# Kernel optimization log

Hardware: AMD Instinct MI355X
Metric: run time of the kernel (lower is better)

Reference implementation:

```python
import jax, jax.numpy as jnp
import numpy as np
from jax import lax

D_MODEL = 512
INPUT_DIM = 64
D_INNER = 1024      # expand * d_model
D_STATE = 128
NHEADS = 16         # d_inner // headdim (headdim = ssm_state//num_heads = 64)
HEADDIM = 64
D_CONV = 4
CONV_DIM = D_INNER + 2 * D_STATE          # 1280 (ngroups=1)
D_IN_PROJ = 2 * D_INNER + 2 * D_STATE + NHEADS  # 2320
BATCH = 2
SEQ = 1024
MASK_RATIO = 0.75
EPS = 1e-5


def setup_inputs() -> dict:
    key = jax.random.key(0)
    ks = jax.random.split(key, 14)
    s = lambda fan: 1.0 / np.sqrt(fan)
    return {
        "x": jax.random.normal(ks[0], (BATCH, SEQ, INPUT_DIM), jnp.float32),
        "conv_emb_w": jax.random.normal(ks[1], (D_MODEL, INPUT_DIM, 3), jnp.float32) * s(INPUT_DIM * 3),
        "conv_emb_b": jax.random.normal(ks[2], (D_MODEL,), jnp.float32) * 0.02,
        "cls_token": jax.random.normal(ks[3], (1, 1, D_MODEL), jnp.float32) * 0.02,
        "in_proj_w": jax.random.normal(ks[4], (D_IN_PROJ, D_MODEL), jnp.float32) * s(D_MODEL),
        "conv1d_w": jax.random.normal(ks[5], (CONV_DIM, 1, D_CONV), jnp.float32) * s(D_CONV),
        "conv1d_b": jax.random.normal(ks[6], (CONV_DIM,), jnp.float32) * 0.02,
        "dt_bias": jax.random.uniform(ks[7], (NHEADS,), jnp.float32, -4.0, 0.0),
        "A_log": jnp.log(jax.random.uniform(ks[8], (NHEADS,), jnp.float32, 1.0, 16.0)),
        "D": jax.random.normal(ks[9], (NHEADS,), jnp.float32),
        "rms_w": jnp.ones((D_INNER,), jnp.float32),
        "out_proj_w": jax.random.normal(ks[10], (D_MODEL, D_INNER), jnp.float32) * s(D_INNER),
        "ln_g": jnp.ones((D_MODEL,), jnp.float32),
        "ln_b": jnp.zeros((D_MODEL,), jnp.float32),
    }


def _forward(x, conv_emb_w, conv_emb_b, cls_token, in_proj_w, conv1d_w, conv1d_b,
             dt_bias, A_log, D, rms_w, out_proj_w, ln_g, ln_b):
    b = x.shape[0]
    # ---- conv embedding: Conv1d(k=3, pad=1) over time ----
    xe = lax.conv_general_dilated(x.transpose(0, 2, 1), conv_emb_w, (1,), [(1, 1)],
                                  dimension_numbers=("NCH", "OIH", "NCH"))
    xe = (xe + conv_emb_b[None, :, None]).transpose(0, 2, 1)  # (b, L, d_model)
    # ---- append CLS token at end ----
    h = jnp.concatenate([xe, jnp.broadcast_to(cls_token, (b, 1, D_MODEL))], axis=1)
    L = h.shape[1]
    # ---- Mamba2 block ----
    zxbcdt = jnp.einsum("bld,ed->ble", h, in_proj_w)  # (b, L, 2320)
    z = zxbcdt[..., :D_INNER]
    xBC = zxbcdt[..., D_INNER:D_INNER + CONV_DIM]
    dt = jax.nn.softplus(zxbcdt[..., -NHEADS:] + dt_bias)  # (b, L, h)
    # causal depthwise conv (pad left d_conv-1) + SiLU
    xBC = lax.conv_general_dilated(xBC.transpose(0, 2, 1), conv1d_w, (1,), [(D_CONV - 1, 0)],
                                   dimension_numbers=("NCH", "OIH", "NCH"),
                                   feature_group_count=CONV_DIM)
    xBC = jax.nn.silu((xBC + conv1d_b[None, :, None]).transpose(0, 2, 1))  # (b, L, 1280)
    x_in = xBC[..., :D_INNER].reshape(b, L, NHEADS, HEADDIM)   # (b, L, h, p)
    B = xBC[..., D_INNER:D_INNER + D_STATE]                     # (b, L, n)
    C = xBC[..., D_INNER + D_STATE:]                            # (b, L, n)
    A = -jnp.exp(A_log)                                         # (h,)
    dA = jnp.exp(dt * A)                                        # (b, L, h)
    # selective state-space scan; state (b, h, p, n)
    def step(state, inp):
        x_t, dt_t, B_t, C_t, dA_t = inp  # (b,h,p) (b,h) (b,n) (b,n) (b,h)
        state = state * dA_t[:, :, None, None] + \
            (dt_t[:, :, None] * x_t)[..., None] * B_t[:, None, None, :]
        y_t = jnp.einsum("bhpn,bn->bhp", state, C_t)
        return state, y_t
    s0 = jnp.zeros((b, NHEADS, HEADDIM, D_STATE), x.dtype)
    _, ys = lax.scan(step, s0, (x_in.transpose(1, 0, 2, 3), dt.transpose(1, 0, 2),
                                B.transpose(1, 0, 2), C.transpose(1, 0, 2),
                                dA.transpose(1, 0, 2)))
    y = ys.transpose(1, 0, 2, 3) + D[None, None, :, None] * x_in  # (b, L, h, p)
    y = y.reshape(b, L, D_INNER)
    # gated RMSNorm: gate first, then normalize
    y = y * jax.nn.silu(z)
    y = y * lax.rsqrt(jnp.mean(y * y, axis=-1, keepdims=True) + EPS) * rms_w
    out = jnp.einsum("ble,de->bld", y, out_proj_w)  # (b, L, d_model)
    # ---- LayerNorm ----
    mu = jnp.mean(out, axis=-1, keepdims=True)
    var = jnp.mean((out - mu) ** 2, axis=-1, keepdims=True)
    out = (out - mu) * lax.rsqrt(var + EPS) * ln_g + ln_b
    return out


def reference(x, conv_emb_w, conv_emb_b, cls_token, in_proj_w, conv1d_w, conv1d_b,
              dt_bias, A_log, D, rms_w, out_proj_w, ln_g, ln_b):
    out = _forward(x, conv_emb_w, conv_emb_b, cls_token, in_proj_w, conv1d_w, conv1d_b,
                   dt_bias, A_log, D, rms_w, out_proj_w, ln_g, ln_b)
    b = out.shape[0]
    cls = out[:, -1:, :]
    body = out[:, :-1, :]                      # (b, SEQ, d)
    len_keep = int(SEQ * (1 - MASK_RATIO))     # 256
    noise = jax.random.uniform(jax.random.fold_in(jax.random.key(0), 1), (b, SEQ))
    ids_shuffle = jnp.argsort(noise, axis=1)
    ids_restore = jnp.argsort(ids_shuffle, axis=1)
    ids_keep = ids_shuffle[:, :len_keep]
    x_masked = jnp.take_along_axis(body, ids_keep[:, :, None], axis=1)
    mask = jnp.where(jnp.arange(SEQ)[None, :] < len_keep, 0.0, 1.0)
    mask = jnp.take_along_axis(jnp.broadcast_to(mask, (b, SEQ)), ids_restore, axis=1)
    x_out = jnp.concatenate([x_masked, cls], axis=1)  # (b, len_keep+1, d)
    return (x_out, mask, ids_restore, ids_keep)
```

## Files before the change

### kernel.cpp

```cpp
#include <hip/hip_runtime.h>
#include <hip/hip_bf16.h>
#include <stdint.h>

#define LTOK  1025
#define NROWS 2050
#define DM    512
#define DIN   1024
#define DST   128
#define NHEAD 16
#define HDIM  64
#define CDIM  1280
#define EPROJ 2320
#define QC    64
#define NCH   17

#define O_RIDX   0
#define O_CB     1024
#define O_CLS    1536
#define O_C1B    2048
#define O_DTB    3328
#define O_ALOG   3344
#define O_DV     3360
#define O_RMSW   3376
#define O_LNG    4400
#define O_LNB    4912
#define O_CW     5440
#define O_IPW    103744
#define O_OPW    1291584
#define O_C1W    1815872
#define O_CX     1820992
#define O_ZX     1952064
#define O_XBC    6708064
#define O_DT     9332064
#define O_LGA    9364864
#define O_Y      9397664
#define O_H      9397664
#define O_X3     10447264
#define O_OUTG   11496864
#define O_SL     11760032
#define O_CLA    16216480
#define O_SL2    16251296
#define O_KEEP   18479520
#define O_OUTP   18480128

#define OO_MASK 263168
#define OO_IDR  265216
#define OO_IDK  267264

typedef __attribute__((ext_vector_type(8))) short short8;
typedef __attribute__((ext_vector_type(8))) unsigned short ushortx8;
typedef __attribute__((ext_vector_type(4))) short shortx4;
typedef __attribute__((ext_vector_type(4))) float floatx4;

__device__ __forceinline__ short f2bs(float f) {
  union { float f; uint32_t u; } v; v.f = f;
  uint32_t r = (v.u + 0x7FFFu + ((v.u >> 16) & 1u)) >> 16;
  return (short)r;
}
__device__ __forceinline__ float bf2f(uint16_t u) {
  return __uint_as_float(((uint32_t)u) << 16);
}

struct InPtrs { const void* p[14]; };

__device__ __forceinline__ uint32_t rotl32(uint32_t v, int d) {
  return (v << d) | (v >> (32 - d));
}
__device__ void threefry2x32(uint32_t k0, uint32_t k1, uint32_t c0, uint32_t c1,
                             uint32_t& o0, uint32_t& o1) {
  uint32_t ks0 = k0, ks1 = k1, ks2 = 0x1BD11BDAu ^ k0 ^ k1;
  uint32_t x0 = c0 + ks0, x1 = c1 + ks1;
#define TF_R4(a,b,c,d) \
  x0 += x1; x1 = rotl32(x1,a); x1 ^= x0; \
  x0 += x1; x1 = rotl32(x1,b); x1 ^= x0; \
  x0 += x1; x1 = rotl32(x1,c); x1 ^= x0; \
  x0 += x1; x1 = rotl32(x1,d); x1 ^= x0;
  TF_R4(13,15,26,6)  x0 += ks1; x1 += ks2 + 1u;
  TF_R4(17,29,16,24) x0 += ks2; x1 += ks0 + 2u;
  TF_R4(13,15,26,6)  x0 += ks0; x1 += ks1 + 3u;
  TF_R4(17,29,16,24) x0 += ks1; x1 += ks2 + 4u;
  TF_R4(13,15,26,6)  x0 += ks2; x1 += ks0 + 5u;
#undef TF_R4
  o0 = x0; o1 = x1;
}

__device__ int detect_is_f32(const uint32_t* w, int nelem) {
  int nw = nelem / 2; if (nw > 16) nw = 16;
  int insane = 0, lozero = 0, anynz = 0;
  for (int i = 0; i < nw; ++i) {
    uint32_t word = w[i];
    if (word != 0u) anynz = 1;
    uint32_t lo = word & 0xffffu;
    if (lo == 0u) { lozero++; continue; }
    float v = __uint_as_float(lo << 16);
    float a = fabsf(v);
    if (!(a >= 1e-8f && a <= 1e4f)) insane++;
  }
  if (insane >= 2) return 1;
  if (lozero == nw && anynz) return 1;
  return 0;
}

__global__ __launch_bounds__(256) void k_convert(InPtrs ptrs, float* ws,
                                                 float* out, int* rowidx) {
  static const int sizes[13] = {98304, 512, 512, 1187840, 5120, 1280,
                                16, 16, 16, 1024, 524288, 512, 512};
  static const int offs[13]  = {O_CW, O_CB, O_CLS, O_IPW, O_C1W, O_C1B,
                                O_DTB, O_ALOG, O_DV, O_RMSW, O_OPW, O_LNG, O_LNB};
  static const int isbf[13]  = {1,0,0,1,0,0,0,0,0,0,1,0,0};
  int t = blockIdx.y;
  int tid = threadIdx.x;

  if (t >= 14) {
    int b = t - 14;
    int idx = blockIdx.x;
    if (idx > 1024) return;
    if (idx == 1024) {
      const uint32_t* cp = (const uint32_t*)ptrs.p[3];
      __shared__ int cf;
      if (tid == 0) cf = detect_is_f32(cp, 512);
      __syncthreads();
      uint16_t* hout = (uint16_t*)(ws + O_H);
      for (int cch = tid; cch < DM; cch += 256) {
        float v = cf ? ((const float*)cp)[cch] : bf2f(((const uint16_t*)cp)[cch]);
        hout[((long)(b * LTOK + 1024)) * DM + cch] = (uint16_t)f2bs(v);
      }
      return;
    }
    const uint32_t* xp = (const uint32_t*)ptrs.p[0];
    __shared__ int xf;
    if (tid == 0) xf = detect_is_f32(xp, 131072);
    __syncthreads();
    if (tid < 192) {
      int i = tid / 3, k = tid % 3;
      int tt = idx + k - 1;
      float v = 0.f;
      if (tt >= 0 && tt < 1024) {
        long src = ((long)(b * 1024 + tt)) * 64 + i;
        v = xf ? ((const float*)xp)[src] : bf2f(((const uint16_t*)xp)[src]);
      }
      ((uint16_t*)(ws + O_X3))[((long)(b * 1024 + idx)) * 192 + tid] = (uint16_t)f2bs(v);
    }
    return;
  }

  if (t == 13) {
    int bx = blockIdx.x;
    if (bx < 512 || bx >= 544) return;
    int rb = bx - 512;
    int seg = rb & 15, b = rb >> 4;
    uint8_t* keep = (uint8_t*)(ws + O_KEEP);
    __shared__ float vals[1024];
    uint32_t fk0, fk1;
    threefry2x32(0u, 0u, 0u, 1u, fk0, fk1);
#pragma unroll
    for (int k = 0; k < 4; ++k) {
      int i = tid + k * 256;
      uint32_t o0, o1;
      threefry2x32(fk0, fk1, 0u, (uint32_t)(b * 1024 + i), o0, o1);
      uint32_t bits = o0 ^ o1;
      vals[i] = __uint_as_float((bits >> 9) | 0x3f800000u) - 1.0f;
    }
    __syncthreads();
    int tg = seg * 64 + (tid >> 2);
    int qq = tid & 3;
    float v = vals[tg];
    int r = 0;
    int j0 = qq * 256;
    for (int it = 0; it < 256; ++it) {
      int j = j0 + ((it + qq * 8) & 255);
      float vj = vals[j];
      r += (vj < v || (vj == v && j < tg)) ? 1 : 0;
    }
    r += __shfl_xor(r, 1, 64);
    r += __shfl_xor(r, 2, 64);
    if (qq == 0) {
      out[OO_IDR + b * 1024 + tg] = (float)r;
      out[OO_MASK + b * 1024 + tg] = (r < 256) ? 0.0f : 1.0f;
      keep[b * LTOK + tg] = (r < 256) ? 1 : 0;
      if (r < 256) {
        out[OO_IDK + b * 256 + r] = (float)tg;
        rowidx[b * 257 + r] = b * LTOK + tg;
      }
      if (tg == 0) {
        rowidx[b * 257 + 256] = b * LTOK + 1024;
        keep[b * LTOK + 1024] = 1;
      }
    }
    return;
  }

  int n = sizes[t];
  const uint32_t* w = (const uint32_t*)ptrs.p[t + 1];
  __shared__ int sf;
  if (tid == 0) sf = detect_is_f32(w, n);
  __syncthreads();
  int base = (blockIdx.x * 256 + tid) * 4;
  if (base >= n) return;
  if (isbf[t]) {
    ushort4 o;
    if (sf) {
      const float4 vv = *(const float4*)((const float*)w + base);
      o.x = (uint16_t)f2bs(vv.x); o.y = (uint16_t)f2bs(vv.y);
      o.z = (uint16_t)f2bs(vv.z); o.w = (uint16_t)f2bs(vv.w);
    } else {
      const uint32_t* s = w + (base >> 1);
      uint32_t w0 = s[0], w1 = s[1];
      o.x = (uint16_t)(w0 & 0xffffu); o.y = (uint16_t)(w0 >> 16);
      o.z = (uint16_t)(w1 & 0xffffu); o.w = (uint16_t)(w1 >> 16);
    }
    *(ushort4*)((uint16_t*)(ws + offs[t]) + base) = o;
  } else {
    float* dst = ws + offs[t];
    if (sf) {
      *(float4*)(dst + base) = *(const float4*)((const float*)w + base);
    } else {
      const uint32_t* s = w + (base >> 1);
      uint32_t w0 = s[0], w1 = s[1];
      float4 o;
      o.x = __uint_as_float((w0 & 0xffffu) << 16);
      o.y = __uint_as_float(w0 & 0xffff0000u);
      o.z = __uint_as_float((w1 & 0xffffu) << 16);
      o.w = __uint_as_float(w1 & 0xffff0000u);
      *(float4*)(dst + base) = o;
    }
  }
}

__global__ __launch_bounds__(256) void k_cgemm(const uint16_t* __restrict__ A,
                                               const uint16_t* __restrict__ Bw,
                                               uint16_t* __restrict__ H,
                                               const float* __restrict__ bias) {
  __shared__ __align__(16) short sA[64 * 200];
  __shared__ __align__(16) short sB[64 * 200];
  int tid = threadIdx.x;
  int lane = tid & 63, w = tid >> 6;
  int lm = lane & 15, q = lane >> 4;
  int bm = blockIdx.y * 64, bn = blockIdx.x * 64;

#pragma unroll
  for (int it = 0; it < 6; ++it) {
    int li = it * 256 + tid;
    int row = li / 24, col = (li % 24) * 8;
    ushortx8 av = *(const ushortx8*)(A + (long)(bm + row) * 192 + col);
    *(ushortx8*)&sA[row * 200 + col] = av;
    ushortx8 bv = *(const ushortx8*)(Bw + (long)(bn + row) * 192 + col);
    *(ushortx8*)&sB[row * 200 + col] = bv;
  }
  __syncthreads();

  floatx4 acc[4] = {};
#pragma unroll
  for (int kb = 0; kb < 6; ++kb) {
    short8 a = *(const short8*)&sA[(w * 16 + lm) * 200 + kb * 32 + q * 8];
#pragma unroll
    for (int ct = 0; ct < 4; ++ct) {
      short8 b = *(const short8*)&sB[(ct * 16 + lm) * 200 + kb * 32 + q * 8];
      acc[ct] = __builtin_amdgcn_mfma_f32_16x16x32_bf16(a, b, acc[ct], 0, 0, 0);
    }
  }
#pragma unroll
  for (int reg = 0; reg < 4; ++reg) {
    int r = bm + w * 16 + q * 4 + reg;
    long crow = (long)((r >> 10) * LTOK + (r & 1023));
#pragma unroll
    for (int ct = 0; ct < 4; ++ct) {
      int cc = bn + ct * 16 + lm;
      H[crow * DM + cc] = (uint16_t)f2bs(acc[ct][reg] + bias[cc]);
    }
  }
}

__global__ __launch_bounds__(256) void k_ogemm(const uint16_t* __restrict__ A,
                                               const uint16_t* __restrict__ Bw,
                                               float* __restrict__ OUTP) {
  __shared__ __align__(16) short sA[64 * 264];
  __shared__ __align__(16) short sB[64 * 264];
  int tid = threadIdx.x;
  int lane = tid & 63, w = tid >> 6;
  int lm = lane & 15, q = lane >> 4;
  int bm = blockIdx.y * 64, bn = blockIdx.x * 64;
  int kbase = blockIdx.z * 256;

#pragma unroll
  for (int it = 0; it < 8; ++it) {
    int li = it * 256 + tid;
    int row = li >> 5, col = (li & 31) * 8;
    int gm = bm + row;
    ushortx8 av = {0,0,0,0,0,0,0,0};
    if (gm < 514) av = *(const ushortx8*)(A + (long)gm * 1024 + kbase + col);
    *(ushortx8*)&sA[row * 264 + col] = av;
    ushortx8 bv = *(const ushortx8*)(Bw + (long)(bn + row) * 1024 + kbase + col);
    *(ushortx8*)&sB[row * 264 + col] = bv;
  }
  __syncthreads();

  floatx4 acc[4] = {};
#pragma unroll
  for (int kb = 0; kb < 8; ++kb) {
    short8 a = *(const short8*)&sA[(w * 16 + lm) * 264 + kb * 32 + q * 8];
#pragma unroll
    for (int ct = 0; ct < 4; ++ct) {
      short8 b = *(const short8*)&sB[(ct * 16 + lm) * 264 + kb * 32 + q * 8];
      acc[ct] = __builtin_amdgcn_mfma_f32_16x16x32_bf16(a, b, acc[ct], 0, 0, 0);
    }
  }
  float* op = OUTP + (long)blockIdx.z * 263168;
#pragma unroll
  for (int reg = 0; reg < 4; ++reg) {
    int r = bm + w * 16 + q * 4 + reg;
    if (r < 514) {
#pragma unroll
      for (int ct = 0; ct < 4; ++ct)
        op[(long)r * 512 + bn + ct * 16 + lm] = acc[ct][reg];
    }
  }
}

__global__ __launch_bounds__(256) void k_bgemm(
    const void* __restrict__ A, const uint16_t* __restrict__ Bw,
    void* __restrict__ C, const float* __restrict__ bias,
    const int* __restrict__ rowmap, int M, int N, int K, int ldc,
    int cmode, int abf, int obf) {
  __shared__ __align__(16) short sA[2][128 * 40];
  __shared__ __align__(16) short sB[2][128 * 40];
  int tid = threadIdx.x;
  int lane = tid & 63, w = tid >> 6;
  int lm = lane & 15, q = lane >> 4;
  int wm = (w >> 1) * 64, wn = (w & 1) * 64;
  int bm = blockIdx.y * 128, bn = blockIdx.x * 128;
  int gz = gridDim.z;
  int Ks = K / gz;
  int kbase = blockIdx.z * Ks;
  int nk = Ks >> 5;

  int srow[4], scol[4];
  long aoff[4]; bool aok[4]; long boff[4]; bool bok[4];
#pragma unroll
  for (int it = 0; it < 4; ++it) {
    int e4 = (tid + it * 256) * 4;
    srow[it] = e4 >> 5; scol[it] = e4 & 31;
    int gm = bm + srow[it];
    aok[it] = gm < M;
    aoff[it] = aok[it] ? (long)(rowmap ? rowmap[gm] : gm) * K : 0;
    int gn = bn + srow[it];
    bok[it] = gn < N;
    boff[it] = bok[it] ? (long)gn * K : 0;
  }

  auto gload = [&](int kt, float4* vaf, ushort4* vau, ushort4* vb) {
    int kc = kbase + kt * 32;
#pragma unroll
    for (int it = 0; it < 4; ++it) {
      if (abf) {
        if (aok[it]) vau[it] = *(const ushort4*)((const uint16_t*)A + aoff[it] + kc + scol[it]);
        else { vau[it].x = 0; vau[it].y = 0; vau[it].z = 0; vau[it].w = 0; }
      } else {
        vaf[it] = aok[it] ? *(const float4*)((const float*)A + aoff[it] + kc + scol[it])
                          : make_float4(0.f, 0.f, 0.f, 0.f);
      }
      if (bok[it]) vb[it] = *(const ushort4*)(Bw + boff[it] + kc + scol[it]);
      else { vb[it].x = 0; vb[it].y = 0; vb[it].z = 0; vb[it].w = 0; }
    }
  };
  auto sstore = [&](int buf, const float4* vaf, const ushort4* vau, const ushort4* vb) {
#pragma unroll
    for (int it = 0; it < 4; ++it) {
      if (abf)
        *(ushort4*)&sA[buf][srow[it] * 40 + scol[it]] = vau[it];
      else
        *(shortx4*)&sA[buf][srow[it] * 40 + scol[it]] =
            shortx4{f2bs(vaf[it].x), f2bs(vaf[it].y), f2bs(vaf[it].z), f2bs(vaf[it].w)};
      *(ushort4*)&sB[buf][srow[it] * 40 + scol[it]] = vb[it];
    }
  };

  floatx4 acc[4][4] = {};
  float4 vaf[4], naf[4];
  ushort4 vau[4], nau[4], vb[4], nb[4];

  gload(0, vaf, vau, vb);
  sstore(0, vaf, vau, vb);
  for (int kt = 0; kt < nk; ++kt) {
    int cur = kt & 1;
    if (kt + 1 < nk) gload(kt + 1, naf, nau, nb);
    __syncthreads();
    short8 afrag[4], bfrag[4];
#pragma unroll
    for (int i = 0; i < 4; ++i)
      afrag[i] = *(const short8*)&sA[cur][(wm + i * 16 + lm) * 40 + q * 8];
#pragma unroll
    for (int j = 0; j < 4; ++j)
      bfrag[j] = *(const short8*)&sB[cur][(wn + j * 16 + lm) * 40 + q * 8];
#pragma unroll
    for (int i = 0; i < 4; ++i)
#pragma unroll
      for (int j = 0; j < 4; ++j)
        acc[i][j] = __builtin_amdgcn_mfma_f32_16x16x32_bf16(afrag[i], bfrag[j], acc[i][j], 0, 0, 0);
    if (kt + 1 < nk) sstore(1 - cur, naf, nau, nb);
  }

#pragma unroll
  for (int i = 0; i < 4; ++i) {
    int rowl = wm + i * 16 + q * 4;
#pragma unroll
    for (int reg = 0; reg < 4; ++reg) {
      int r = bm + rowl + reg;
      if (r >= M) continue;
      long crow = cmode ? (long)((r >> 10) * LTOK + (r & 1023)) : (long)r;
#pragma unroll
      for (int j = 0; j < 4; ++j) {
        int ccol = bn + wn + j * 16 + lm;
        if (ccol < N) {
          float v = acc[i][j][reg];
          if (gz > 1) {
            atomicAdd(&((float*)C)[crow * ldc + ccol], v);
          } else {
            if (bias) v += bias[ccol];
            if (obf) ((uint16_t*)C)[crow * ldc + ccol] = (uint16_t)f2bs(v);
            else ((float*)C)[crow * ldc + ccol] = v;
          }
        }
      }
    }
  }
}

__global__ __launch_bounds__(256) void k_conv1d(const uint16_t* __restrict__ zx,
                                                const float* __restrict__ w,
                                                const float* __restrict__ bias,
                                                uint16_t* __restrict__ xbc,
                                                const float* __restrict__ dtb,
                                                const float* __restrict__ alog,
                                                float* __restrict__ dt,
                                                float* __restrict__ lga) {
  long rp_ = blockIdx.x;
  if (rp_ >= NROWS) {
    int idx = (int)(rp_ - NROWS) * 256 + threadIdx.x;
    if (idx < NROWS * NHEAD) {
      int rr = idx >> 4, h = idx & 15;
      float xv = bf2f(zx[(long)rr * EPROJ + (EPROJ - NHEAD) + h]) + dtb[h];
      float dtv = (xv > 20.f) ? xv : log1pf(expf(xv));
      dt[idx] = dtv;
      lga[idx] = dtv * (-expf(alog[h]));
    }
    return;
  }
  {
    int xcd = (int)(rp_ & 7), slot = (int)(rp_ >> 3);
    rp_ = (xcd < 2) ? (long)xcd * 257 + slot
                    : (long)514 + (long)(xcd - 2) * 256 + slot;
  }
  long r = rp_;
  int b = (int)(r / LTOK), t = (int)(r % LTOK);
  for (int c4 = threadIdx.x * 4; c4 < CDIM; c4 += 1024) {
    float4 bi = *(const float4*)(bias + c4);
    float a0 = bi.x, a1 = bi.y, a2 = bi.z, a3 = bi.w;
    float4 w0 = *(const float4*)(w + (c4 + 0) * 4);
    float4 w1 = *(const float4*)(w + (c4 + 1) * 4);
    float4 w2 = *(const float4*)(w + (c4 + 2) * 4);
    float4 w3 = *(const float4*)(w + (c4 + 3) * 4);
    float wr0[4] = {w0.x, w0.y, w0.z, w0.w};
    float wr1[4] = {w1.x, w1.y, w1.z, w1.w};
    float wr2[4] = {w2.x, w2.y, w2.z, w2.w};
    float wr3[4] = {w3.x, w3.y, w3.z, w3.w};
#pragma unroll
    for (int k = 0; k < 4; ++k) {
      int tt = t - 3 + k;
      if (tt >= 0) {
        ushort4 xv = *(const ushort4*)(zx + ((long)(b * LTOK + tt)) * EPROJ + DIN + c4);
        a0 = fmaf(wr0[k], bf2f(xv.x), a0);
        a1 = fmaf(wr1[k], bf2f(xv.y), a1);
        a2 = fmaf(wr2[k], bf2f(xv.z), a2);
        a3 = fmaf(wr3[k], bf2f(xv.w), a3);
      }
    }
    ushort4 o;
    o.x = (uint16_t)f2bs(a0 / (1.f + expf(-a0)));
    o.y = (uint16_t)f2bs(a1 / (1.f + expf(-a1)));
    o.z = (uint16_t)f2bs(a2 / (1.f + expf(-a2)));
    o.w = (uint16_t)f2bs(a3 / (1.f + expf(-a3)));
    *(ushort4*)(xbc + r * CDIM + c4) = o;
  }
}

__global__ __launch_bounds__(256) void k_ssd1(const uint16_t* __restrict__ xbc,
                                              const float* __restrict__ dt,
                                              const float* __restrict__ lga,
                                              float* __restrict__ SL,
                                              float* __restrict__ CLA) {
  int blk = blockIdx.x;
  int c = blk % NCH;
  int hh = blk / NCH;
  int h = hh & 15, b = hh >> 4;
  int tid = threadIdx.x;
  int lane = tid & 63, w = tid >> 6;
  int lm = lane & 15, q = lane >> 4;

  __shared__ __align__(16) short sBT[128 * 72];
  __shared__ __align__(16) short sXT[64 * 72];
  __shared__ float wwv[64];

  int t0 = c * QC;
  const uint16_t* base = xbc + (long)b * LTOK * CDIM;

  if (tid < 64) {
    int t = t0 + tid;
    float dtv = (t < LTOK) ? dt[((long)(b * LTOK + t)) * NHEAD + h] : 0.f;
    float v   = (t < LTOK) ? lga[((long)(b * LTOK + t)) * NHEAD + h] : 0.f;
#pragma unroll
    for (int off = 1; off < 64; off <<= 1) {
      float u = __shfl_up(v, off, 64);
      if (lane >= off) v += u;
    }
    float clEnd = __shfl(v, 63, 64);
    wwv[tid] = __expf(clEnd - v) * dtv;
    CLA[(long)blk * 64 + tid] = v;
  }
  __syncthreads();

#pragma unroll
  for (int k = 0; k < 8; ++k) {
    int e4 = (tid + k * 256) * 4;
    int row = e4 >> 7, col = e4 & 127;
    int t = t0 + row;
    ushort4 bv = {0,0,0,0};
    if (t < LTOK) bv = *(const ushort4*)(base + (long)t * CDIM + DIN + col);
    float wv = wwv[row];
    sBT[(col  )*72+row]=f2bs(bf2f(bv.x)*wv); sBT[(col+1)*72+row]=f2bs(bf2f(bv.y)*wv);
    sBT[(col+2)*72+row]=f2bs(bf2f(bv.z)*wv); sBT[(col+3)*72+row]=f2bs(bf2f(bv.w)*wv);
  }
#pragma unroll
  for (int k = 0; k < 4; ++k) {
    int e4 = (tid + k * 256) * 4;
    int row = e4 >> 6, col = e4 & 63;
    int t = t0 + row;
    ushort4 xv = {0,0,0,0};
    if (t < LTOK) xv = *(const ushort4*)(base + (long)t * CDIM + h * 64 + col);
    sXT[(col  )*72+row]=(short)xv.x; sXT[(col+1)*72+row]=(short)xv.y;
    sXT[(col+2)*72+row]=(short)xv.z; sXT[(col+3)*72+row]=(short)xv.w;
  }
  __syncthreads();

  floatx4 s[2][4] = {};
#pragma unroll
  for (int kb = 0; kb < 2; ++kb) {
    short8 bfr[4];
#pragma unroll
    for (int ct = 0; ct < 4; ++ct)
      bfr[ct] = *(const short8*)&sXT[(ct*16 + lm)*72 + kb*32 + q*8];
#pragma unroll
    for (int nt = 0; nt < 2; ++nt) {
      short8 a = *(const short8*)&sBT[((w*2+nt)*16 + lm)*72 + kb*32 + q*8];
#pragma unroll
      for (int ct = 0; ct < 4; ++ct)
        s[nt][ct] = __builtin_amdgcn_mfma_f32_16x16x32_bf16(a, bfr[ct], s[nt][ct], 0, 0, 0);
    }
  }
  float* slp = SL + (long)blk * 8192;
#pragma unroll
  for (int nt = 0; nt < 2; ++nt)
#pragma unroll
    for (int ct = 0; ct < 4; ++ct)
#pragma unroll
      for (int reg = 0; reg < 4; ++reg) {
        int n = (w*2+nt)*16 + q*4 + reg;
        int p = ct*16 + lm;
        slp[n*64 + p] = s[nt][ct][reg];
      }
}

__global__ __launch_bounds__(256) void k_comb(const float* __restrict__ SL,
                                              const float* __restrict__ CLA,
                                              uint16_t* __restrict__ SL2) {
  int bx = blockIdx.x;
  int piece = bx & 15;
  int hh = bx >> 4;
  int off = piece * 512 + threadIdx.x * 2;
  long cb0 = (long)hh * NCH;
  float P[NCH];
  float2 tmp[NCH];
#pragma unroll
  for (int c = 0; c < NCH; ++c) {
    P[c] = __expf(CLA[(cb0 + c) * 64 + 63]);
    tmp[c] = *(const float2*)(SL + (cb0 + c) * 8192 + off);
  }
  float2 s = make_float2(0.f, 0.f);
#pragma unroll
  for (int c = 0; c < NCH; ++c) {
    uint32_t packed = (uint32_t)(uint16_t)f2bs(s.x) | ((uint32_t)(uint16_t)f2bs(s.y) << 16);
    *(uint32_t*)(SL2 + (cb0 + c) * 8192 + off) = packed;
    s.x = fmaf(P[c], s.x, tmp[c].x);
    s.y = fmaf(P[c], s.y, tmp[c].y);
  }
}

__global__ __launch_bounds__(256) void k_ssd3(const uint16_t* __restrict__ xbc,
                                              const float* __restrict__ dt,
                                              const uint16_t* __restrict__ SL2,
                                              const float* __restrict__ CLA,
                                              const uint8_t* __restrict__ keepf,
                                              float* __restrict__ Y) {
  int blk = blockIdx.x;
  int c = blk % NCH;
  int hh = blk / NCH;
  int h = hh & 15, b = hh >> 4;
  int tid = threadIdx.x;
  int lane = tid & 63, w = tid >> 6;
  int lm = lane & 15, q = lane >> 4;

  __shared__ __align__(16) short sST[64 * 136];
  __shared__ __align__(16) short sXT[64 * 72];
  __shared__ __align__(16) short sM[64 * 72];
  __shared__ float dtw[64], clA[64], evec[64];
  __shared__ uint8_t kf[64];

  int t0 = c * QC;
  const uint16_t* base = xbc + (long)b * LTOK * CDIM;
  const uint16_t* slp = SL2 + (long)blk * 8192;

  if (tid < 64) {
    int t = t0 + tid;
    dtw[tid] = (t < LTOK) ? dt[((long)(b * LTOK + t)) * NHEAD + h] : 0.f;
    float v = CLA[(long)blk * 64 + tid];
    clA[tid] = v;
    evec[tid] = __expf(v);
    kf[tid] = (t < LTOK) ? keepf[b * LTOK + t] : 0;
  }

#pragma unroll
  for (int k = 0; k < 4; ++k) {
    int e4 = (tid + k * 256) * 4;
    int row = e4 >> 6, col = e4 & 63;
    int t = t0 + row;
    ushort4 xv = {0,0,0,0};
    if (t < LTOK) xv = *(const ushort4*)(base + (long)t * CDIM + h * 64 + col);
    sXT[(col  )*72+row]=(short)xv.x; sXT[(col+1)*72+row]=(short)xv.y;
    sXT[(col+2)*72+row]=(short)xv.z; sXT[(col+3)*72+row]=(short)xv.w;
  }
#pragma unroll
  for (int k = 0; k < 8; ++k) {
    int e4 = (tid + k * 256) * 4;
    int n = e4 >> 6, p = e4 & 63;
    ushort4 sv = *(const ushort4*)(slp + n * 64 + p);
    sST[(p  )*136+n]=(short)sv.x; sST[(p+1)*136+n]=(short)sv.y;
    sST[(p+2)*136+n]=(short)sv.z; sST[(p+3)*136+n]=(short)sv.w;
  }
  __syncthreads();

  short8 cfr[4];
  int tA = t0 + w*16 + lm;
  bool tAok = tA < LTOK;
#pragma unroll
  for (int kb = 0; kb < 4; ++kb) {
    short8 z = {0,0,0,0,0,0,0,0};
    cfr[kb] = tAok ? *(const short8*)(base + (long)tA * CDIM + DIN + DST + kb*32 + q*8) : z;
  }

  floatx4 g[4] = {};
#pragma unroll
  for (int kb = 0; kb < 4; ++kb) {
#pragma unroll
    for (int ct = 0; ct < 4; ++ct) {
      int tB = t0 + ct*16 + lm;
      short8 z = {0,0,0,0,0,0,0,0};
      short8 bb = (tB < LTOK) ? *(const short8*)(base + (long)tB * CDIM + DIN + kb*32 + q*8) : z;
      g[ct] = __builtin_amdgcn_mfma_f32_16x16x32_bf16(cfr[kb], bb, g[ct], 0, 0, 0);
    }
  }
#pragma unroll
  for (int ct = 0; ct < 4; ++ct) {
    int tp = ct*16 + lm;
#pragma unroll
    for (int reg = 0; reg < 4; ++reg) {
      int tl = w*16 + q*4 + reg;
      float m = 0.f;
      if (tp <= tl) m = g[ct][reg] * __expf(clA[tl] - clA[tp]) * dtw[tp];
      sM[tl*72 + tp] = f2bs(m);
    }
  }
  floatx4 y2[4] = {};
#pragma unroll
  for (int kb = 0; kb < 4; ++kb) {
#pragma unroll
    for (int ct = 0; ct < 4; ++ct) {
      short8 bb = *(const short8*)&sST[(ct*16 + lm)*136 + kb*32 + q*8];
      y2[ct] = __builtin_amdgcn_mfma_f32_16x16x32_bf16(cfr[kb], bb, y2[ct], 0, 0, 0);
    }
  }
  __syncthreads();
  floatx4 y1[4] = {};
#pragma unroll
  for (int kb = 0; kb < 2; ++kb) {
    short8 a = *(const short8*)&sM[(w*16 + lm)*72 + kb*32 + q*8];
#pragma unroll
    for (int ct = 0; ct < 4; ++ct) {
      short8 bb = *(const short8*)&sXT[(ct*16 + lm)*72 + kb*32 + q*8];
      y1[ct] = __builtin_amdgcn_mfma_f32_16x16x32_bf16(a, bb, y1[ct], 0, 0, 0);
    }
  }
#pragma unroll
  for (int reg = 0; reg < 4; ++reg) {
    int tl = w*16 + q*4 + reg;
    int t = t0 + tl;
    if (t < LTOK && kf[tl]) {
      float ev = evec[tl];
#pragma unroll
      for (int ct = 0; ct < 4; ++ct) {
        int p = ct*16 + lm;
        Y[((long)(b * LTOK + t)) * DIN + h * 64 + p] = y1[ct][reg] + ev * y2[ct][reg];
      }
    }
  }
}

__global__ __launch_bounds__(256) void k_gaterms(const float* __restrict__ Y,
                                                 const uint16_t* __restrict__ xbc,
                                                 const uint16_t* __restrict__ zx,
                                                 const float* __restrict__ Dv,
                                                 const float* __restrict__ rmsw,
                                                 const int* __restrict__ ridx,
                                                 uint16_t* __restrict__ G) {
  int rr = blockIdx.x;
  long r = ridx[rr];
  int tid = threadIdx.x;
  int e = tid * 4;
  int h = tid >> 4;
  float4 a = *(const float4*)(Y + r * DIN + e);
  const ushort4 xu = *(const ushort4*)(xbc + r * CDIM + e);
  const ushort4 zu = *(const ushort4*)(zx + r * EPROJ + e);
  float Dh = Dv[h];
  float y0 = a.x + Dh * bf2f(xu.x), y1 = a.y + Dh * bf2f(xu.y);
  float y2 = a.z + Dh * bf2f(xu.z), y3 = a.w + Dh * bf2f(xu.w);
  float z0 = bf2f(zu.x), z1 = bf2f(zu.y), z2 = bf2f(zu.z), z3 = bf2f(zu.w);
  float g0 = y0 * (z0 / (1.f + expf(-z0)));
  float g1 = y1 * (z1 / (1.f + expf(-z1)));
  float g2 = y2 * (z2 / (1.f + expf(-z2)));
  float g3 = y3 * (z3 / (1.f + expf(-z3)));
  __shared__ float red[256];
  red[tid] = g0*g0 + g1*g1 + g2*g2 + g3*g3;
  __syncthreads();
  for (int st = 128; st; st >>= 1) {
    if (tid < st) red[tid] += red[tid + st];
    __syncthreads();
  }
  float scale = rsqrtf(red[0] * (1.0f / 1024.0f) + 1e-5f);
  float4 rw = *(const float4*)(rmsw + e);
  ushort4 o;
  o.x = (uint16_t)f2bs(g0 * scale * rw.x);
  o.y = (uint16_t)f2bs(g1 * scale * rw.y);
  o.z = (uint16_t)f2bs(g2 * scale * rw.z);
  o.w = (uint16_t)f2bs(g3 * scale * rw.w);
  *(ushort4*)(G + (long)rr * DIN + e) = o;
}

__global__ __launch_bounds__(256) void k_ln(const float* __restrict__ outp,
                                            const float* __restrict__ lng,
                                            const float* __restrict__ lnb,
                                            float* __restrict__ out) {
  int r = blockIdx.x;
  int tid = threadIdx.x;
  long e = (long)r * DM + tid * 2;
  float2 v0 = *(const float2*)(outp + e);
  float2 v1 = *(const float2*)(outp + 263168 + e);
  float2 v2 = *(const float2*)(outp + 2 * 263168 + e);
  float2 v3 = *(const float2*)(outp + 3 * 263168 + e);
  float2 v;
  v.x = ((v0.x + v1.x) + v2.x) + v3.x;
  v.y = ((v0.y + v1.y) + v2.y) + v3.y;
  __shared__ float red[256];
  red[tid] = v.x + v.y;
  __syncthreads();
  for (int st = 128; st; st >>= 1) { if (tid < st) red[tid] += red[tid + st]; __syncthreads(); }
  float mu = red[0] * (1.0f / 512.0f);
  __syncthreads();
  float dx = v.x - mu, dy = v.y - mu;
  red[tid] = dx * dx + dy * dy;
  __syncthreads();
  for (int st = 128; st; st >>= 1) { if (tid < st) red[tid] += red[tid + st]; __syncthreads(); }
  float sc = rsqrtf(red[0] * (1.0f / 512.0f) + 1e-5f);
  int c = tid * 2;
  out[(long)r * DM + c]     = dx * sc * lng[c] + lnb[c];
  out[(long)r * DM + c + 1] = dy * sc * lng[c + 1] + lnb[c + 1];
}

extern "C" void kernel_launch(void* const* d_in, const int* in_sizes, int n_in,
                              void* d_out, int out_size, void* d_ws, size_t ws_size,
                              hipStream_t stream) {
  float* ws = (float*)d_ws;
  float* out = (float*)d_out;
  int* rowidx = (int*)(ws + O_RIDX);
  InPtrs ip;
  for (int i = 0; i < 14; ++i) ip.p[i] = d_in[i];

  hipLaunchKernelGGL(k_convert, dim3(1160, 16), dim3(256), 0, stream, ip, ws, out, rowidx);
  hipLaunchKernelGGL(k_cgemm, dim3(8, 32), dim3(256), 0, stream,
                     (const uint16_t*)(ws + O_X3), (const uint16_t*)(ws + O_CW),
                     (uint16_t*)(ws + O_H), ws + O_CB);
  hipLaunchKernelGGL(k_bgemm, dim3(19, 17, 1), dim3(256), 0, stream,
                     (const void*)(ws + O_H), (const uint16_t*)(ws + O_IPW),
                     (void*)(ws + O_ZX), (const float*)nullptr, (const int*)nullptr,
                     2050, 2320, 512, 2320, 0, 1, 1);
  hipLaunchKernelGGL(k_conv1d, dim3(2179), dim3(256), 0, stream,
                     (const uint16_t*)(ws + O_ZX), ws + O_C1W, ws + O_C1B,
                     (uint16_t*)(ws + O_XBC),
                     ws + O_DTB, ws + O_ALOG, ws + O_DT, ws + O_LGA);
  hipLaunchKernelGGL(k_ssd1, dim3(32 * NCH), dim3(256), 0, stream,
                     (const uint16_t*)(ws + O_XBC), ws + O_DT, ws + O_LGA,
                     ws + O_SL, ws + O_CLA);
  hipLaunchKernelGGL(k_comb, dim3(512), dim3(256), 0, stream,
                     ws + O_SL, ws + O_CLA, (uint16_t*)(ws + O_SL2));
  hipLaunchKernelGGL(k_ssd3, dim3(32 * NCH), dim3(256), 0, stream,
                     (const uint16_t*)(ws + O_XBC), ws + O_DT,
                     (const uint16_t*)(ws + O_SL2), ws + O_CLA,
                     (const uint8_t*)(ws + O_KEEP), ws + O_Y);
  hipLaunchKernelGGL(k_gaterms, dim3(514), dim3(256), 0, stream,
                     ws + O_Y, (const uint16_t*)(ws + O_XBC),
                     (const uint16_t*)(ws + O_ZX), ws + O_DV, ws + O_RMSW,
                     (const int*)rowidx, (uint16_t*)(ws + O_X3));
  hipLaunchKernelGGL(k_ogemm, dim3(8, 9, 4), dim3(256), 0, stream,
                     (const uint16_t*)(ws + O_X3), (const uint16_t*)(ws + O_OPW),
                     ws + O_OUTP);
  hipLaunchKernelGGL(k_ln, dim3(514), dim3(256), 0, stream,
                     ws + O_OUTP, ws + O_LNG, ws + O_LNB, out);
}
```

Before: 199.9 us.

## Fold conv embedding into in_proj weights to fuse the two GEMMs

Precomputes a combined weight W2 = in_proj_w · conv_emb_w (2320x192) plus a folded bias and the CLS row projection, then runs a single K=192 GEMM from the im2col input straight into zxbcdt. This drops the intermediate H tensor and the K=512 in_proj GEMM over 2050 rows, trading them for a small weight-fold GEMM run on every call. Rounding changes because the product of weights is rounded to bf16 before use, and the CLS row is now computed separately.

```diff
diff --git a/kernel.cpp b/kernel.cpp
--- a/kernel.cpp
+++ b/kernel.cpp
@@ -34,7 +34,6 @@
 #define O_DT     9332064
 #define O_LGA    9364864
 #define O_Y      9397664
-#define O_H      9397664
 #define O_X3     10447264
 #define O_OUTG   11496864
 #define O_SL     11760032
@@ -42,6 +41,9 @@
 #define O_SL2    16251296
 #define O_KEEP   18479520
 #define O_OUTP   18480128
+#define O_CWT    19532800
+#define O_W2     19581952
+#define O_BIAS2  19804672
 
 #define OO_MASK 263168
 #define OO_IDR  265216
@@ -114,19 +116,7 @@
   if (t >= 14) {
     int b = t - 14;
     int idx = blockIdx.x;
-    if (idx > 1024) return;
-    if (idx == 1024) {
-      const uint32_t* cp = (const uint32_t*)ptrs.p[3];
-      __shared__ int cf;
-      if (tid == 0) cf = detect_is_f32(cp, 512);
-      __syncthreads();
-      uint16_t* hout = (uint16_t*)(ws + O_H);
-      for (int cch = tid; cch < DM; cch += 256) {
-        float v = cf ? ((const float*)cp)[cch] : bf2f(((const uint16_t*)cp)[cch]);
-        hout[((long)(b * LTOK + 1024)) * DM + cch] = (uint16_t)f2bs(v);
-      }
-      return;
-    }
+    if (idx >= 1024) return;
     const uint32_t* xp = (const uint32_t*)ptrs.p[0];
     __shared__ int xf;
     if (tid == 0) xf = detect_is_f32(xp, 131072);
@@ -190,6 +180,32 @@
     return;
   }
 
+  if (t == 0) {
+    const uint32_t* w = (const uint32_t*)ptrs.p[1];
+    __shared__ int sf;
+    if (tid == 0) sf = detect_is_f32(w, 98304);
+    __syncthreads();
+    int base = (blockIdx.x * 256 + tid) * 4;
+    if (base >= 98304) return;
+    uint16_t vv[4];
+    if (sf) {
+      const float4 f = *(const float4*)((const float*)w + base);
+      vv[0] = (uint16_t)f2bs(f.x); vv[1] = (uint16_t)f2bs(f.y);
+      vv[2] = (uint16_t)f2bs(f.z); vv[3] = (uint16_t)f2bs(f.w);
+    } else {
+      const uint32_t* s = w + (base >> 1);
+      uint32_t w0 = s[0], w1 = s[1];
+      vv[0] = (uint16_t)(w0 & 0xffffu); vv[1] = (uint16_t)(w0 >> 16);
+      vv[2] = (uint16_t)(w1 & 0xffffu); vv[3] = (uint16_t)(w1 >> 16);
+    }
+    int o = base / 192, ik = base % 192;
+    uint16_t* cwt = (uint16_t*)(ws + O_CWT);
+#pragma unroll
+    for (int j = 0; j < 4; ++j)
+      cwt[(long)(ik + j) * 512 + o] = vv[j];
+    return;
+  }
+
   int n = sizes[t];
   const uint32_t* w = (const uint32_t*)ptrs.p[t + 1];
   __shared__ int sf;
@@ -227,24 +243,105 @@
   }
 }
 
-__global__ __launch_bounds__(256) void k_cgemm(const uint16_t* __restrict__ A,
-                                               const uint16_t* __restrict__ Bw,
-                                               uint16_t* __restrict__ H,
-                                               const float* __restrict__ bias) {
+__global__ __launch_bounds__(256) void k_w2(const uint16_t* __restrict__ IPW,
+                                            const uint16_t* __restrict__ CWT,
+                                            const float* __restrict__ cb,
+                                            const float* __restrict__ cls,
+                                            uint16_t* __restrict__ W2,
+                                            float* __restrict__ bias2,
+                                            uint16_t* __restrict__ ZX) {
+  int bx = blockIdx.x;
+  int tid = threadIdx.x;
+
+  if (bx >= 111) {
+    __shared__ float scb[512];
+    __shared__ float scl[512];
+    for (int i = tid; i < 512; i += 256) {
+      scb[i] = cb[i];
+      scl[i] = bf2f((uint16_t)f2bs(cls[i]));
+    }
+    __syncthreads();
+    int e = (bx - 111) * 232 + tid;
+    if (tid < 232 && e < 2320) {
+      float sb = 0.f, sc = 0.f;
+      for (int d8 = 0; d8 < 512; d8 += 8) {
+        ushortx8 v = *(const ushortx8*)(IPW + (long)e * 512 + d8);
+#pragma unroll
+        for (int j = 0; j < 8; ++j) {
+          float wv = bf2f(v[j]);
+          sb = fmaf(wv, scb[d8 + j], sb);
+          sc = fmaf(wv, scl[d8 + j], sc);
+        }
+      }
+      bias2[e] = sb;
+      uint16_t cz = (uint16_t)f2bs(sc);
+      ZX[(long)1024 * EPROJ + e] = cz;
+      ZX[(long)2049 * EPROJ + e] = cz;
+    }
+    return;
+  }
+
+  int bm = bx / 3, bn = bx % 3;
+  __shared__ __align__(16) short sA[64 * 136];
+  __shared__ __align__(16) short sB[64 * 136];
+  int lane = tid & 63, w = tid >> 6, lm = lane & 15, q = lane >> 4;
+
+  floatx4 acc[4] = {};
+  for (int ph = 0; ph < 4; ++ph) {
+    int d0 = ph * 128;
+#pragma unroll
+    for (int it = 0; it < 4; ++it) {
+      int li = it * 256 + tid;
+      int row = li >> 4, col = (li & 15) * 8;
+      int ge = bm * 64 + row;
+      ushortx8 av = {0,0,0,0,0,0,0,0};
+      if (ge < 2320) av = *(const ushortx8*)(IPW + (long)ge * 512 + d0 + col);
+      *(ushortx8*)&sA[row * 136 + col] = av;
+      ushortx8 bv = *(const ushortx8*)(CWT + (long)(bn * 64 + row) * 512 + d0 + col);
+      *(ushortx8*)&sB[row * 136 + col] = bv;
+    }
+    __syncthreads();
+#pragma unroll
+    for (int kk = 0; kk < 4; ++kk) {
+      short8 a = *(const short8*)&sA[(w * 16 + lm) * 136 + kk * 32 + q * 8];
+#pragma unroll
+      for (int ct = 0; ct < 4; ++ct) {
+        short8 b = *(const short8*)&sB[(ct * 16 + lm) * 136 + kk * 32 + q * 8];
+        acc[ct] = __builtin_amdgcn_mfma_f32_16x16x32_bf16(a, b, acc[ct], 0, 0, 0);
+      }
+    }
+    __syncthreads();
+  }
+#pragma unroll
+  for (int reg = 0; reg < 4; ++reg) {
+    int e = bm * 64 + w * 16 + q * 4 + reg;
+    if (e < 2320) {
+#pragma unroll
+      for (int ct = 0; ct < 4; ++ct)
+        W2[(long)e * 192 + bn * 64 + ct * 16 + lm] = (uint16_t)f2bs(acc[ct][reg]);
+    }
+  }
+}
+
+__global__ __launch_bounds__(256) void k_ipgemm(const uint16_t* __restrict__ X3,
+                                                const uint16_t* __restrict__ W2,
+                                                const float* __restrict__ bias2,
+                                                uint16_t* __restrict__ ZX) {
   __shared__ __align__(16) short sA[64 * 200];
   __shared__ __align__(16) short sB[64 * 200];
   int tid = threadIdx.x;
-  int lane = tid & 63, w = tid >> 6;
-  int lm = lane & 15, q = lane >> 4;
+  int lane = tid & 63, w = tid >> 6, lm = lane & 15, q = lane >> 4;
   int bm = blockIdx.y * 64, bn = blockIdx.x * 64;
 
 #pragma unroll
   for (int it = 0; it < 6; ++it) {
     int li = it * 256 + tid;
     int row = li / 24, col = (li % 24) * 8;
-    ushortx8 av = *(const ushortx8*)(A + (long)(bm + row) * 192 + col);
+    ushortx8 av = *(const ushortx8*)(X3 + (long)(bm + row) * 192 + col);
     *(ushortx8*)&sA[row * 200 + col] = av;
-    ushortx8 bv = *(const ushortx8*)(Bw + (long)(bn + row) * 192 + col);
+    int gn = bn + row;
+    ushortx8 bv = {0,0,0,0,0,0,0,0};
+    if (gn < 2320) bv = *(const ushortx8*)(W2 + (long)gn * 192 + col);
     *(ushortx8*)&sB[row * 200 + col] = bv;
   }
   __syncthreads();
@@ -265,163 +362,9 @@
     long crow = (long)((r >> 10) * LTOK + (r & 1023));
 #pragma unroll
     for (int ct = 0; ct < 4; ++ct) {
-      int cc = bn + ct * 16 + lm;
-      H[crow * DM + cc] = (uint16_t)f2bs(acc[ct][reg] + bias[cc]);
-    }
-  }
-}
-
-__global__ __launch_bounds__(256) void k_ogemm(const uint16_t* __restrict__ A,
-                                               const uint16_t* __restrict__ Bw,
-                                               float* __restrict__ OUTP) {
-  __shared__ __align__(16) short sA[64 * 264];
-  __shared__ __align__(16) short sB[64 * 264];
-  int tid = threadIdx.x;
-  int lane = tid & 63, w = tid >> 6;
-  int lm = lane & 15, q = lane >> 4;
-  int bm = blockIdx.y * 64, bn = blockIdx.x * 64;
-  int kbase = blockIdx.z * 256;
-
-#pragma unroll
-  for (int it = 0; it < 8; ++it) {
-    int li = it * 256 + tid;
-    int row = li >> 5, col = (li & 31) * 8;
-    int gm = bm + row;
-    ushortx8 av = {0,0,0,0,0,0,0,0};
-    if (gm < 514) av = *(const ushortx8*)(A + (long)gm * 1024 + kbase + col);
-    *(ushortx8*)&sA[row * 264 + col] = av;
-    ushortx8 bv = *(const ushortx8*)(Bw + (long)(bn + row) * 1024 + kbase + col);
-    *(ushortx8*)&sB[row * 264 + col] = bv;
-  }
-  __syncthreads();
-
-  floatx4 acc[4] = {};
-#pragma unroll
-  for (int kb = 0; kb < 8; ++kb) {
-    short8 a = *(const short8*)&sA[(w * 16 + lm) * 264 + kb * 32 + q * 8];
-#pragma unroll
-    for (int ct = 0; ct < 4; ++ct) {
-      short8 b = *(const short8*)&sB[(ct * 16 + lm) * 264 + kb * 32 + q * 8];
-      acc[ct] = __builtin_amdgcn_mfma_f32_16x16x32_bf16(a, b, acc[ct], 0, 0, 0);
-    }
-  }
-  float* op = OUTP + (long)blockIdx.z * 263168;
-#pragma unroll
-  for (int reg = 0; reg < 4; ++reg) {
-    int r = bm + w * 16 + q * 4 + reg;
-    if (r < 514) {
-#pragma unroll
-      for (int ct = 0; ct < 4; ++ct)
-        op[(long)r * 512 + bn + ct * 16 + lm] = acc[ct][reg];
-    }
-  }
-}
-
-__global__ __launch_bounds__(256) void k_bgemm(
-    const void* __restrict__ A, const uint16_t* __restrict__ Bw,
-    void* __restrict__ C, const float* __restrict__ bias,
-    const int* __restrict__ rowmap, int M, int N, int K, int ldc,
-    int cmode, int abf, int obf) {
-  __shared__ __align__(16) short sA[2][128 * 40];
-  __shared__ __align__(16) short sB[2][128 * 40];
-  int tid = threadIdx.x;
-  int lane = tid & 63, w = tid >> 6;
-  int lm = lane & 15, q = lane >> 4;
-  int wm = (w >> 1) * 64, wn = (w & 1) * 64;
-  int bm = blockIdx.y * 128, bn = blockIdx.x * 128;
-  int gz = gridDim.z;
-  int Ks = K / gz;
-  int kbase = blockIdx.z * Ks;
-  int nk = Ks >> 5;
-
-  int srow[4], scol[4];
-  long aoff[4]; bool aok[4]; long boff[4]; bool bok[4];
-#pragma unroll
-  for (int it = 0; it < 4; ++it) {
-    int e4 = (tid + it * 256) * 4;
-    srow[it] = e4 >> 5; scol[it] = e4 & 31;
-    int gm = bm + srow[it];
-    aok[it] = gm < M;
-    aoff[it] = aok[it] ? (long)(rowmap ? rowmap[gm] : gm) * K : 0;
-    int gn = bn + srow[it];
-    bok[it] = gn < N;
-    boff[it] = bok[it] ? (long)gn * K : 0;
-  }
-
-  auto gload = [&](int kt, float4* vaf, ushort4* vau, ushort4* vb) {
-    int kc = kbase + kt * 32;
-#pragma unroll
-    for (int it = 0; it < 4; ++it) {
-      if (abf) {
-        if (aok[it]) vau[it] = *(const ushort4*)((const uint16_t*)A + aoff[it] + kc + scol[it]);
-        else { vau[it].x = 0; vau[it].y = 0; vau[it].z = 0; vau[it].w = 0; }
-      } else {
-        vaf[it] = aok[it] ? *(const float4*)((const float*)A + aoff[it] + kc + scol[it])
-                          : make_float4(0.f, 0.f, 0.f, 0.f);
-      }
-      if (bok[it]) vb[it] = *(const ushort4*)(Bw + boff[it] + kc + scol[it]);
-      else { vb[it].x = 0; vb[it].y = 0; vb[it].z = 0; vb[it].w = 0; }
-    }
-  };
-  auto sstore = [&](int buf, const float4* vaf, const ushort4* vau, const ushort4* vb) {
-#pragma unroll
-    for (int it = 0; it < 4; ++it) {
-      if (abf)
-        *(ushort4*)&sA[buf][srow[it] * 40 + scol[it]] = vau[it];
-      else
-        *(shortx4*)&sA[buf][srow[it] * 40 + scol[it]] =
-            shortx4{f2bs(vaf[it].x), f2bs(vaf[it].y), f2bs(vaf[it].z), f2bs(vaf[it].w)};
-      *(ushort4*)&sB[buf][srow[it] * 40 + scol[it]] = vb[it];
-    }
-  };
-
-  floatx4 acc[4][4] = {};
-  float4 vaf[4], naf[4];
-  ushort4 vau[4], nau[4], vb[4], nb[4];
-
-  gload(0, vaf, vau, vb);
-  sstore(0, vaf, vau, vb);
-  for (int kt = 0; kt < nk; ++kt) {
-    int cur = kt & 1;
-    if (kt + 1 < nk) gload(kt + 1, naf, nau, nb);
-    __syncthreads();
-    short8 afrag[4], bfrag[4];
-#pragma unroll
-    for (int i = 0; i < 4; ++i)
-      afrag[i] = *(const short8*)&sA[cur][(wm + i * 16 + lm) * 40 + q * 8];
-#pragma unroll
-    for (int j = 0; j < 4; ++j)
-      bfrag[j] = *(const short8*)&sB[cur][(wn + j * 16 + lm) * 40 + q * 8];
-#pragma unroll
-    for (int i = 0; i < 4; ++i)
-#pragma unroll
-      for (int j = 0; j < 4; ++j)
-        acc[i][j] = __builtin_amdgcn_mfma_f32_16x16x32_bf16(afrag[i], bfrag[j], acc[i][j], 0, 0, 0);
-    if (kt + 1 < nk) sstore(1 - cur, naf, nau, nb);
-  }
-
-#pragma unroll
-  for (int i = 0; i < 4; ++i) {
-    int rowl = wm + i * 16 + q * 4;
-#pragma unroll
-    for (int reg = 0; reg < 4; ++reg) {
-      int r = bm + rowl + reg;
-      if (r >= M) continue;
-      long crow = cmode ? (long)((r >> 10) * LTOK + (r & 1023)) : (long)r;
-#pragma unroll
-      for (int j = 0; j < 4; ++j) {
-        int ccol = bn + wn + j * 16 + lm;
-        if (ccol < N) {
-          float v = acc[i][j][reg];
-          if (gz > 1) {
-            atomicAdd(&((float*)C)[crow * ldc + ccol], v);
-          } else {
-            if (bias) v += bias[ccol];
-            if (obf) ((uint16_t*)C)[crow * ldc + ccol] = (uint16_t)f2bs(v);
-            else ((float*)C)[crow * ldc + ccol] = v;
-          }
-        }
-      }
+      int e = bn + ct * 16 + lm;
+      if (e < 2320)
+        ZX[crow * EPROJ + e] = (uint16_t)f2bs(acc[ct][reg] + bias2[e]);
     }
   }
 }
@@ -754,6 +697,52 @@
   *(ushort4*)(G + (long)rr * DIN + e) = o;
 }
 
+__global__ __launch_bounds__(256) void k_ogemm(const uint16_t* __restrict__ A,
+                                               const uint16_t* __restrict__ Bw,
+                                               float* __restrict__ OUTP) {
+  __shared__ __align__(16) short sA[64 * 264];
+  __shared__ __align__(16) short sB[64 * 264];
+  int tid = threadIdx.x;
+  int lane = tid & 63, w = tid >> 6;
+  int lm = lane & 15, q = lane >> 4;
+  int bm = blockIdx.y * 64, bn = blockIdx.x * 64;
+  int kbase = blockIdx.z * 256;
+
+#pragma unroll
+  for (int it = 0; it < 8; ++it) {
+    int li = it * 256 + tid;
+    int row = li >> 5, col = (li & 31) * 8;
+    int gm = bm + row;
+    ushortx8 av = {0,0,0,0,0,0,0,0};
+    if (gm < 514) av = *(const ushortx8*)(A + (long)gm * 1024 + kbase + col);
+    *(ushortx8*)&sA[row * 264 + col] = av;
+    ushortx8 bv = *(const ushortx8*)(Bw + (long)(bn + row) * 1024 + kbase + col);
+    *(ushortx8*)&sB[row * 264 + col] = bv;
+  }
+  __syncthreads();
+
+  floatx4 acc[4] = {};
+#pragma unroll
+  for (int kb = 0; kb < 8; ++kb) {
+    short8 a = *(const short8*)&sA[(w * 16 + lm) * 264 + kb * 32 + q * 8];
+#pragma unroll
+    for (int ct = 0; ct < 4; ++ct) {
+      short8 b = *(const short8*)&sB[(ct * 16 + lm) * 264 + kb * 32 + q * 8];
+      acc[ct] = __builtin_amdgcn_mfma_f32_16x16x32_bf16(a, b, acc[ct], 0, 0, 0);
+    }
+  }
+  float* op = OUTP + (long)blockIdx.z * 263168;
+#pragma unroll
+  for (int reg = 0; reg < 4; ++reg) {
+    int r = bm + w * 16 + q * 4 + reg;
+    if (r < 514) {
+#pragma unroll
+      for (int ct = 0; ct < 4; ++ct)
+        op[(long)r * 512 + bn + ct * 16 + lm] = acc[ct][reg];
+    }
+  }
+}
+
 __global__ __launch_bounds__(256) void k_ln(const float* __restrict__ outp,
                                             const float* __restrict__ lng,
                                             const float* __restrict__ lnb,
@@ -794,13 +783,13 @@
   for (int i = 0; i < 14; ++i) ip.p[i] = d_in[i];
 
   hipLaunchKernelGGL(k_convert, dim3(1160, 16), dim3(256), 0, stream, ip, ws, out, rowidx);
-  hipLaunchKernelGGL(k_cgemm, dim3(8, 32), dim3(256), 0, stream,
-                     (const uint16_t*)(ws + O_X3), (const uint16_t*)(ws + O_CW),
-                     (uint16_t*)(ws + O_H), ws + O_CB);
-  hipLaunchKernelGGL(k_bgemm, dim3(19, 17, 1), dim3(256), 0, stream,
-                     (const void*)(ws + O_H), (const uint16_t*)(ws + O_IPW),
-                     (void*)(ws + O_ZX), (const float*)nullptr, (const int*)nullptr,
-                     2050, 2320, 512, 2320, 0, 1, 1);
+  hipLaunchKernelGGL(k_w2, dim3(121), dim3(256), 0, stream,
+                     (const uint16_t*)(ws + O_IPW), (const uint16_t*)(ws + O_CWT),
+                     ws + O_CB, ws + O_CLS,
+                     (uint16_t*)(ws + O_W2), ws + O_BIAS2, (uint16_t*)(ws + O_ZX));
+  hipLaunchKernelGGL(k_ipgemm, dim3(37, 32), dim3(256), 0, stream,
+                     (const uint16_t*)(ws + O_X3), (const uint16_t*)(ws + O_W2),
+                     ws + O_BIAS2, (uint16_t*)(ws + O_ZX));
   hipLaunchKernelGGL(k_conv1d, dim3(2179), dim3(256), 0, stream,
                      (const uint16_t*)(ws + O_ZX), ws + O_C1W, ws + O_C1B,
                      (uint16_t*)(ws + O_XBC),
```

After: 199.1 us. No clear change (-0.4%).
